# Kernel tuning notes

Measured on AMD Instinct MI355X. Metric: run time of the kernel, lower is better.

The kernel has to match this reference:

```python
import jax, jax.numpy as jnp
import numpy as np

D_ENC = 512
D_DEC = 512
JOINT = 512
VOCAB = 1024


def setup_inputs() -> dict:
    key = jax.random.key(0)
    ks = jax.random.split(key, 7)
    B, T, U = 4, 256, 64
    s_enc = 1.0 / np.sqrt(D_ENC)
    s_dec = 1.0 / np.sqrt(D_DEC)
    s_out = 1.0 / np.sqrt(JOINT)
    return {
        "encoder_out": jax.random.normal(ks[0], (B, T, 1, D_ENC), dtype=jnp.float32),
        "decoder_out": jax.random.normal(ks[1], (B, 1, U, D_DEC), dtype=jnp.float32),
        # torch.nn.Linear stores weight as (out, in); uniform(-1/sqrt(in), 1/sqrt(in))
        "W_enc": jax.random.uniform(ks[2], (JOINT, D_ENC), jnp.float32, -s_enc, s_enc),
        "b_enc": jax.random.uniform(ks[3], (JOINT,), jnp.float32, -s_enc, s_enc),
        "W_dec": jax.random.uniform(ks[4], (JOINT, D_DEC), jnp.float32, -s_dec, s_dec),
        "W_out": jax.random.uniform(ks[5], (VOCAB, JOINT), jnp.float32, -s_out, s_out),
        "b_out": jax.random.uniform(ks[6], (VOCAB,), jnp.float32, -s_out, s_out),
    }


def reference(encoder_out, decoder_out, W_enc, b_enc, W_dec, W_out, b_out):
    # Project each side in its small shape first (B,T,1,J) and (B,1,U,J),
    # then broadcast-add over (T,U), tanh, output GEMM -> (B,T,U,V).
    enc = jnp.einsum("btud,jd->btuj", encoder_out, W_enc) + b_enc  # (B,T,1,J)
    dec = jnp.einsum("btud,jd->btuj", decoder_out, W_dec)          # (B,1,U,J)
    h = jnp.tanh(enc + dec)                                        # (B,T,U,J)
    return jnp.einsum("btuj,vj->btuv", h, W_out) + b_out           # (B,T,U,V)
```

## Files before the change

### kernel.cpp

```cpp
#include <hip/hip_runtime.h>
#include <hip/hip_bf16.h>


typedef __attribute__((ext_vector_type(8))) short short8;
typedef __attribute__((ext_vector_type(4))) float f32x4;
typedef __attribute__((ext_vector_type(16))) float f32x16;

#define SZ0 524288
#define SZ1 131072
#define SZ2 262144
#define SZ3 512
#define SZ4 262144
#define SZ5 524288
#define SZ6 1024
#define CU0 0
#define CU1 524288
#define CU2 655360
#define CU3 917504
#define CU4 918016
#define CU5 1180160
#define CU6 1704448
#define CTOT 1705472

__global__ void detect_kernel(const void* p0, const void* p1, const void* p2,
                              const void* p3, const void* p4, const void* p5,
                              const void* p6, int* flags) {
  const void* ps[7] = {p0, p1, p2, p3, p4, p5, p6};
  const int sz[7] = {SZ0, SZ1, SZ2, SZ3, SZ4, SZ5, SZ6};
  const int w = threadIdx.x >> 6;
  const int l = threadIdx.x & 63;
  if (w >= 7) return;
  const unsigned short* u = (const unsigned short*)ps[w];
  const int lim = sz[w] < 1024 ? sz[w] : 1024;
  int bad = 0;
  for (int j = l; j < lim; j += 64) {
    const unsigned e = (u[j] >> 7) & 0xFFu;
    if (e >= 0x8Eu) bad = 1;
  }
  const unsigned long long b = __ballot(bad);
  if (l == 0) flags[w] = (b != 0ULL) ? 1 : 0;
}

__global__ __launch_bounds__(256) void convert_kernel(
    const void* p0, const void* p1, const void* p2, const void* p3,
    const void* p4, const void* p5, const void* p6,
    const int* __restrict__ flags, __hip_bfloat16* __restrict__ dst) {
  const int gid = blockIdx.x * 256 + threadIdx.x;
  if (gid >= CTOT) return;
  int t, local;
  const void* p;
  if (gid < CU1)      { t = 0; local = gid - CU0; p = p0; }
  else if (gid < CU2) { t = 1; local = gid - CU1; p = p1; }
  else if (gid < CU3) { t = 2; local = gid - CU2; p = p2; }
  else if (gid < CU4) { t = 3; local = gid - CU3; p = p3; }
  else if (gid < CU5) { t = 4; local = gid - CU4; p = p4; }
  else if (gid < CU6) { t = 5; local = gid - CU5; p = p5; }
  else                { t = 6; local = gid - CU6; p = p6; }
  __hip_bfloat16 v;
  if (flags[t])
    v = __float2bfloat16(((const float*)p)[local]);
  else
    v = ((const __hip_bfloat16*)p)[local];
  dst[gid] = v;
}

__device__ __forceinline__ void gemm_bt_body(
    const __hip_bfloat16* __restrict__ A, const __hip_bfloat16* __restrict__ Bw,
    const __hip_bfloat16* __restrict__ bias, float* __restrict__ C,
    int M, int N, int K, int bid,
    __hip_bfloat16* sA, __hip_bfloat16* sB) {
  const int tid = threadIdx.x;
  const int w = tid >> 6;
  const int l = tid & 63;
  const int ntiles = N >> 7;
  const int mt = bid / ntiles;
  const int nt = bid % ntiles;
  const int m0 = mt << 7;
  const int n0 = nt << 7;
  const int wm = (w >> 1) << 6;
  const int wn = (w & 1) << 6;
  const int r16 = l & 15;
  const int q = l >> 4;

  f32x4 acc[4][4] = {};

  const int srow_in = l >> 3;
  const int scol = (l & 7) << 3;

  for (int k0 = 0; k0 < K; k0 += 64) {
#pragma unroll
    for (int i = 0; i < 4; ++i) {
      const int c = (w << 2) + i;
      const int row = (c << 3) + srow_in;
      const __hip_bfloat16* gA = A + (size_t)(m0 + row) * K + k0 + scol;
      const __hip_bfloat16* gB = Bw + (size_t)(n0 + row) * K + k0 + scol;
      __builtin_amdgcn_global_load_lds(
          (const __attribute__((address_space(1))) void*)gA,
          (__attribute__((address_space(3))) void*)(sA + (c << 9) + (l << 3)),
          16, 0, 0);
      __builtin_amdgcn_global_load_lds(
          (const __attribute__((address_space(1))) void*)gB,
          (__attribute__((address_space(3))) void*)(sB + (c << 9) + (l << 3)),
          16, 0, 0);
    }
    __syncthreads();

#pragma unroll
    for (int kk = 0; kk < 2; ++kk) {
      const int kc = (kk << 5) + (q << 3);
      short8 af[4], bf[4];
#pragma unroll
      for (int mi = 0; mi < 4; ++mi)
        af[mi] = *(const short8*)(sA + (wm + (mi << 4) + r16) * 64 + kc);
#pragma unroll
      for (int ni = 0; ni < 4; ++ni)
        bf[ni] = *(const short8*)(sB + (wn + (ni << 4) + r16) * 64 + kc);
#pragma unroll
      for (int mi = 0; mi < 4; ++mi)
#pragma unroll
        for (int ni = 0; ni < 4; ++ni)
          acc[mi][ni] = __builtin_amdgcn_mfma_f32_16x16x32_bf16(
              af[mi], bf[ni], acc[mi][ni], 0, 0, 0);
    }
    __syncthreads();
  }

#pragma unroll
  for (int ni = 0; ni < 4; ++ni) {
    const int col = n0 + wn + (ni << 4) + r16;
    const float bc = bias ? __bfloat162float(bias[col]) : 0.0f;
#pragma unroll
    for (int mi = 0; mi < 4; ++mi) {
      const int rowb = m0 + wm + (mi << 4) + (q << 2);
#pragma unroll
      for (int i = 0; i < 4; ++i)
        C[(size_t)(rowb + i) * N + col] = acc[mi][ni][i] + bc;
    }
  }
}

__global__ __launch_bounds__(256) void proj_kernel(
    const __hip_bfloat16* __restrict__ enc, const __hip_bfloat16* __restrict__ Wenc,
    const __hip_bfloat16* __restrict__ benc,
    const __hip_bfloat16* __restrict__ dec, const __hip_bfloat16* __restrict__ Wdec,
    float* __restrict__ Pe, float* __restrict__ Pd) {
  __shared__ __align__(16) __hip_bfloat16 sA[128 * 64];
  __shared__ __align__(16) __hip_bfloat16 sB[128 * 64];
  if (blockIdx.x < 32)
    gemm_bt_body(enc, Wenc, benc, Pe, 1024, 512, 512, blockIdx.x, sA, sB);
  else
    gemm_bt_body(dec, Wdec, nullptr, Pd, 256, 512, 512, blockIdx.x - 32, sA, sB);
}

__global__ __launch_bounds__(1024, 4) void gemm_joint(
    const float* __restrict__ Pe, const float* __restrict__ Pd,
    const __hip_bfloat16* __restrict__ Bw,
    const __hip_bfloat16* __restrict__ bias, float* __restrict__ out) {
  __shared__ __align__(16) __hip_bfloat16 sH[128 * 512];
  __shared__ __align__(16) __hip_bfloat16 sB[2 * 8192];

  const int t = threadIdx.x;
  const int w = t >> 6;
  const int l = t & 63;
  const int l31 = l & 31;
  const int q2 = l >> 5;
  const int m0 = blockIdx.x << 7;

  auto stage = [&](int iter, int buf) {
    const int n0 = (iter >> 5) << 9;
    const int k0 = (iter & 31) << 4;
    const int n = t & 511;
    const int c = t >> 9;
    const __hip_bfloat16* src = Bw + (size_t)(n0 + n) * 512 + k0 + (c << 3);
    __builtin_amdgcn_global_load_lds(
        (const __attribute__((address_space(1))) void*)src,
        (__attribute__((address_space(3))) void*)(sB + (buf << 13) + (t << 3)),
        16, 0, 0);
  };

  stage(0, 0);

  {
    const int r = t & 127;
    const int seg = t >> 7;
    const int e = (blockIdx.x << 1) + (r >> 6);
    const int d = ((blockIdx.x >> 7) << 6) | (r & 63);
    const float* pe = Pe + (size_t)e * 512 + (seg << 6);
    const float* pd = Pd + (size_t)d * 512 + (seg << 6);
    const int swr = r & 63;
#pragma unroll
    for (int i = 0; i < 8; ++i) {
      const int cc = (seg << 3) + i;
      const f32x4 a0 = *(const f32x4*)(pe + (i << 3));
      const f32x4 a1 = *(const f32x4*)(pe + (i << 3) + 4);
      const f32x4 b0 = *(const f32x4*)(pd + (i << 3));
      const f32x4 b1 = *(const f32x4*)(pd + (i << 3) + 4);
      short8 hv;
#pragma unroll
      for (int jj = 0; jj < 4; ++jj) {
        float s = a0[jj] + b0[jj];
        float tv = 1.0f - 2.0f / (__expf(2.0f * s) + 1.0f);
        __hip_bfloat16 hb = __float2bfloat16(tv);
        hv[jj] = *(const short*)&hb;
        s = a1[jj] + b1[jj];
        tv = 1.0f - 2.0f / (__expf(2.0f * s) + 1.0f);
        hb = __float2bfloat16(tv);
        hv[4 + jj] = *(const short*)&hb;
      }
      *(short8*)(sH + (r << 9) + ((cc ^ swr) << 3)) = hv;
    }
  }
  __syncthreads();

  const int wm = (w >> 3) << 6;
  const int wn = (w & 7) << 6;
  f32x16 acc[2][2] = {};

  int arow[2], aswz[2];
#pragma unroll
  for (int mi = 0; mi < 2; ++mi) {
    const int row = wm + (mi << 5) + l31;
    arow[mi] = row << 9;
    aswz[mi] = row & 63;
  }
  int boff[2];
#pragma unroll
  for (int ni = 0; ni < 2; ++ni)
    boff[ni] = (q2 << 12) + ((wn + (ni << 5) + l31) << 3);

  int buf = 0;
  for (int iter = 0; iter < 64; ++iter) {
    if (iter < 63) stage(iter + 1, buf ^ 1);

    const int cb = ((iter & 31) << 1) + q2;
    short8 af[2], bf[2];
#pragma unroll
    for (int mi = 0; mi < 2; ++mi)
      af[mi] = *(const short8*)(sH + arow[mi] + ((cb ^ aswz[mi]) << 3));
#pragma unroll
    for (int ni = 0; ni < 2; ++ni)
      bf[ni] = *(const short8*)(sB + (buf << 13) + boff[ni]);
#pragma unroll
    for (int mi = 0; mi < 2; ++mi)
#pragma unroll
      for (int ni = 0; ni < 2; ++ni)
        acc[mi][ni] = __builtin_amdgcn_mfma_f32_32x32x16_bf16(
            af[mi], bf[ni], acc[mi][ni], 0, 0, 0);

    if ((iter & 31) == 31) {
      const int n0 = (iter >> 5) << 9;
#pragma unroll
      for (int ni = 0; ni < 2; ++ni) {
        const int col = n0 + wn + (ni << 5) + l31;
        const float bc = __bfloat162float(bias[col]);
#pragma unroll
        for (int mi = 0; mi < 2; ++mi) {
#pragma unroll
          for (int rr = 0; rr < 16; ++rr) {
            const int row = m0 + wm + (mi << 5) + (rr & 3) + ((rr >> 2) << 3) +
                            (q2 << 2);
            out[(size_t)row * 1024 + col] = acc[mi][ni][rr] + bc;
          }
          acc[mi][ni] = (f32x16){};
        }
      }
    }

    __syncthreads();
    buf ^= 1;
  }
}

extern "C" void kernel_launch(void* const* d_in, const int* in_sizes, int n_in,
                              void* d_out, int out_size, void* d_ws,
                              size_t ws_size, hipStream_t stream) {
  char* ws = (char*)d_ws;
  int* flags = (int*)ws;
  __hip_bfloat16* cp = (__hip_bfloat16*)(ws + 256);
  float* Pe = (float*)(ws + (4ull << 20));
  float* Pd = (float*)(ws + (6ull << 20));

  detect_kernel<<<dim3(1), dim3(512), 0, stream>>>(
      d_in[0], d_in[1], d_in[2], d_in[3], d_in[4], d_in[5], d_in[6], flags);
  convert_kernel<<<dim3((CTOT + 255) / 256), dim3(256), 0, stream>>>(
      d_in[0], d_in[1], d_in[2], d_in[3], d_in[4], d_in[5], d_in[6], flags, cp);

  const __hip_bfloat16* enc_c = cp + CU0;
  const __hip_bfloat16* dec_c = cp + CU1;
  const __hip_bfloat16* Wenc_c = cp + CU2;
  const __hip_bfloat16* benc_c = cp + CU3;
  const __hip_bfloat16* Wdec_c = cp + CU4;
  const __hip_bfloat16* Wout_c = cp + CU5;
  const __hip_bfloat16* bout_c = cp + CU6;

  proj_kernel<<<dim3(40), dim3(256), 0, stream>>>(enc_c, Wenc_c, benc_c,
                                                  dec_c, Wdec_c, Pe, Pd);
  gemm_joint<<<dim3(512), dim3(1024), 0, stream>>>(
      Pe, Pd, Wout_c, bout_c, (float*)d_out);
}
```

Before: 482.4 us.

## Retile joint GEMM to 64-row blocks covering full vocab per block

New measurement: 472.9 us. -2.0%, faster.

```diff
diff --git a/kernel.cpp b/kernel.cpp
--- a/kernel.cpp
+++ b/kernel.cpp
@@ -152,42 +152,42 @@
     gemm_bt_body(dec, Wdec, nullptr, Pd, 256, 512, 512, blockIdx.x - 32, sA, sB);
 }
 
-__global__ __launch_bounds__(1024, 4) void gemm_joint(
+__global__ __launch_bounds__(512, 2) void gemm_joint(
     const float* __restrict__ Pe, const float* __restrict__ Pd,
     const __hip_bfloat16* __restrict__ Bw,
     const __hip_bfloat16* __restrict__ bias, float* __restrict__ out) {
-  __shared__ __align__(16) __hip_bfloat16 sH[128 * 512];
-  __shared__ __align__(16) __hip_bfloat16 sB[2 * 8192];
+  __shared__ __align__(16) __hip_bfloat16 sH[64 * 512];
+  __shared__ __align__(16) __hip_bfloat16 sB[2 * 16384];
 
   const int t = threadIdx.x;
   const int w = t >> 6;
   const int l = t & 63;
   const int l31 = l & 31;
   const int q2 = l >> 5;
-  const int m0 = blockIdx.x << 7;
-
-  auto stage = [&](int iter, int buf) {
-    const int n0 = (iter >> 5) << 9;
-    const int k0 = (iter & 31) << 4;
-    const int n = t & 511;
-    const int c = t >> 9;
-    const __hip_bfloat16* src = Bw + (size_t)(n0 + n) * 512 + k0 + (c << 3);
-    __builtin_amdgcn_global_load_lds(
-        (const __attribute__((address_space(1))) void*)src,
-        (__attribute__((address_space(3))) void*)(sB + (buf << 13) + (t << 3)),
-        16, 0, 0);
+  const int m0 = blockIdx.x << 6;
+
+  auto stage = [&](int ks, int bufbit) {
+#pragma unroll
+    for (int h = 0; h < 4; ++h) {
+      const int n = (w << 7) + (h << 5) + (l >> 1);
+      const __hip_bfloat16* src =
+          Bw + (size_t)n * 512 + (ks << 4) + ((l & 1) << 3);
+      __builtin_amdgcn_global_load_lds(
+          (const __attribute__((address_space(1))) void*)src,
+          (__attribute__((address_space(3))) void*)(
+              sB + (bufbit << 14) + ((((w << 2) + h) << 9) + (l << 3))),
+          16, 0, 0);
+    }
   };
 
   stage(0, 0);
 
   {
-    const int r = t & 127;
-    const int seg = t >> 7;
-    const int e = (blockIdx.x << 1) + (r >> 6);
-    const int d = ((blockIdx.x >> 7) << 6) | (r & 63);
-    const float* pe = Pe + (size_t)e * 512 + (seg << 6);
+    const int r = l;
+    const int seg = w;
+    const int d = ((blockIdx.x >> 8) << 6) | r;
+    const float* pe = Pe + (size_t)blockIdx.x * 512 + (seg << 6);
     const float* pd = Pd + (size_t)d * 512 + (seg << 6);
-    const int swr = r & 63;
 #pragma unroll
     for (int i = 0; i < 8; ++i) {
       const int cc = (seg << 3) + i;
@@ -207,67 +207,62 @@
         hb = __float2bfloat16(tv);
         hv[4 + jj] = *(const short*)&hb;
       }
-      *(short8*)(sH + (r << 9) + ((cc ^ swr) << 3)) = hv;
+      *(short8*)(sH + (r << 9) + ((cc ^ r) << 3)) = hv;
     }
   }
   __syncthreads();
 
-  const int wm = (w >> 3) << 6;
-  const int wn = (w & 7) << 6;
-  f32x16 acc[2][2] = {};
-
-  int arow[2], aswz[2];
-#pragma unroll
-  for (int mi = 0; mi < 2; ++mi) {
-    const int row = wm + (mi << 5) + l31;
-    arow[mi] = row << 9;
-    aswz[mi] = row & 63;
-  }
-  int boff[2];
-#pragma unroll
-  for (int ni = 0; ni < 2; ++ni)
-    boff[ni] = (q2 << 12) + ((wn + (ni << 5) + l31) << 3);
-
-  int buf = 0;
-  for (int iter = 0; iter < 64; ++iter) {
-    if (iter < 63) stage(iter + 1, buf ^ 1);
-
-    const int cb = ((iter & 31) << 1) + q2;
-    short8 af[2], bf[2];
+  const int wn = w << 7;
+  f32x16 acc[2][4] = {};
+
+  for (int ks = 0; ks < 32; ++ks) {
+    const int bufbit = ks & 1;
+    if (ks < 31) {
+      stage(ks + 1, bufbit ^ 1);
+      asm volatile("s_waitcnt vmcnt(4)" ::: "memory");
+    } else {
+      asm volatile("s_waitcnt vmcnt(0)" ::: "memory");
+    }
+    __builtin_amdgcn_sched_barrier(0);
+    __builtin_amdgcn_s_barrier();
+    __builtin_amdgcn_sched_barrier(0);
+
+    const int cb = (ks << 1) + q2;
+    short8 af[2];
+#pragma unroll
+    for (int mi = 0; mi < 2; ++mi) {
+      const int r = (mi << 5) + l31;
+      af[mi] = *(const short8*)(sH + (r << 9) + ((cb ^ r) << 3));
+    }
+    short8 bf[4];
+#pragma unroll
+    for (int ni = 0; ni < 4; ++ni)
+      bf[ni] = *(const short8*)(sB + (bufbit << 14) +
+                                ((wn + (ni << 5) + l31) << 4) + (q2 << 3));
 #pragma unroll
     for (int mi = 0; mi < 2; ++mi)
-      af[mi] = *(const short8*)(sH + arow[mi] + ((cb ^ aswz[mi]) << 3));
-#pragma unroll
-    for (int ni = 0; ni < 2; ++ni)
-      bf[ni] = *(const short8*)(sB + (buf << 13) + boff[ni]);
-#pragma unroll
-    for (int mi = 0; mi < 2; ++mi)
-#pragma unroll
-      for (int ni = 0; ni < 2; ++ni)
+#pragma unroll
+      for (int ni = 0; ni < 4; ++ni)
         acc[mi][ni] = __builtin_amdgcn_mfma_f32_32x32x16_bf16(
             af[mi], bf[ni], acc[mi][ni], 0, 0, 0);
 
-    if ((iter & 31) == 31) {
-      const int n0 = (iter >> 5) << 9;
-#pragma unroll
-      for (int ni = 0; ni < 2; ++ni) {
-        const int col = n0 + wn + (ni << 5) + l31;
-        const float bc = __bfloat162float(bias[col]);
-#pragma unroll
-        for (int mi = 0; mi < 2; ++mi) {
-#pragma unroll
-          for (int rr = 0; rr < 16; ++rr) {
-            const int row = m0 + wm + (mi << 5) + (rr & 3) + ((rr >> 2) << 3) +
-                            (q2 << 2);
-            out[(size_t)row * 1024 + col] = acc[mi][ni][rr] + bc;
-          }
-          acc[mi][ni] = (f32x16){};
-        }
+    __builtin_amdgcn_sched_barrier(0);
+    __builtin_amdgcn_s_barrier();
+    __builtin_amdgcn_sched_barrier(0);
+  }
+
+#pragma unroll
+  for (int ni = 0; ni < 4; ++ni) {
+    const int col = wn + (ni << 5) + l31;
+    const float bc = __bfloat162float(bias[col]);
+#pragma unroll
+    for (int mi = 0; mi < 2; ++mi) {
+#pragma unroll
+      for (int rr = 0; rr < 16; ++rr) {
+        const int row = m0 + (mi << 5) + (rr & 3) + ((rr >> 2) << 3) + (q2 << 2);
+        out[(size_t)row * 1024 + col] = acc[mi][ni][rr] + bc;
       }
     }
-
-    __syncthreads();
-    buf ^= 1;
   }
 }
 
@@ -295,6 +290,6 @@
 
   proj_kernel<<<dim3(40), dim3(256), 0, stream>>>(enc_c, Wenc_c, benc_c,
                                                   dec_c, Wdec_c, Pe, Pd);
-  gemm_joint<<<dim3(512), dim3(1024), 0, stream>>>(
+  gemm_joint<<<dim3(1024), dim3(512), 0, stream>>>(
       Pe, Pd, Wout_c, bout_c, (float*)d_out);
 }
```
